# Kernel optimization log

Measured on AMD Instinct MI355X. Metric: run time of the kernel, lower is better.

## Reference

```python
import jax, jax.numpy as jnp
import numpy as np

D_MODEL = 768
N_HEAD = 8
D_K = D_MODEL // N_HEAD
SCALE = float(np.sqrt(D_K))
NEG = -1e9


def setup_inputs() -> dict:
    key = jax.random.key(0)
    ks = jax.random.split(key, 8)
    B, S = 2, 2048
    q = jax.random.normal(ks[0], (B, S, D_MODEL), dtype=jnp.float32)
    k = jax.random.normal(ks[1], (B, S, D_MODEL), dtype=jnp.float32)
    v = jax.random.normal(ks[2], (B, S, D_MODEL), dtype=jnp.float32)
    mask = jax.random.randint(ks[3], (B, 1, S, S), 0, 2, dtype=jnp.int32)
    # nn.Linear(d, d, bias=False) weights, stored as [in, out] for x @ W
    init = 1.0 / np.sqrt(D_MODEL)
    Wq = jax.random.uniform(ks[4], (D_MODEL, D_MODEL), jnp.float32, -init, init)
    Wk = jax.random.uniform(ks[5], (D_MODEL, D_MODEL), jnp.float32, -init, init)
    Wv = jax.random.uniform(ks[6], (D_MODEL, D_MODEL), jnp.float32, -init, init)
    Wo = jax.random.uniform(ks[7], (D_MODEL, D_MODEL), jnp.float32, -init, init)
    return {"query": q, "key": k, "value": v, "mask": mask,
            "Wq": Wq, "Wk": Wk, "Wv": Wv, "Wo": Wo}


def _split_heads(x):
    B, S, _ = x.shape
    return x.reshape(B, S, N_HEAD, D_K).transpose(0, 2, 1, 3)  # [B,H,S,Dk]


def reference(query, key, value, mask, Wq, Wk, Wv, Wo):
    Q = _split_heads(query @ Wq)
    K = _split_heads(key @ Wk)
    V = _split_heads(value @ Wv)
    logits = jnp.einsum('bhqd,bhkd->bhqk', Q, K) / SCALE  # [B,H,S,S]
    logits = jnp.where(mask == 0, NEG, logits)
    attn = jax.nn.softmax(logits, axis=-1)
    x = jnp.einsum('bhqk,bhkd->bhqd', attn, V)  # dropout=0 (eval)
    B, H, S, Dk = x.shape
    concat = x.transpose(0, 2, 1, 3).reshape(B, S, H * Dk)
    return concat @ Wo, attn
```

## Files before the change

### kernel.cpp

```cpp
#include <hip/hip_runtime.h>
#include <hip/hip_bf16.h>

typedef __bf16 bf16_t;
typedef __bf16 bf16x4 __attribute__((ext_vector_type(4)));
typedef __bf16 bf16x8 __attribute__((ext_vector_type(8)));
typedef float f32x4 __attribute__((ext_vector_type(4)));
typedef unsigned long long u64;

#define MFMA16(a, b, c) __builtin_amdgcn_mfma_f32_16x16x32_bf16(a, b, c, 0, 0, 0)

constexpr int B_ = 2, S_ = 2048, DM = 768, H_ = 8, DK = 96;
constexpr size_t OUT_ELEMS = 3145728;
constexpr float INV_SCALE = 0.10206207261596575f;
constexpr float NEGINF = -1e9f;

constexpr size_t QW_OFF = 0, KW_OFF = 6291456, VT_OFF = 12582912, WT_OFF = 18874368;
constexpr size_t XC_OFF = 23592960, MB_OFF = 29884416;

__global__ __launch_bounds__(256) void pack_mask(const int* __restrict__ mask,
                                                 u64* __restrict__ bits) {
    const int row = blockIdx.x;
    const int tid = threadIdx.x, lane = tid & 63, wv = tid >> 6;
    const int* mrow = mask + (size_t)row * S_;
    u64* brow = bits + (size_t)row * 32;
#pragma unroll
    for (int p = 0; p < 8; ++p) {
        const u64 b = __ballot(mrow[p * 256 + wv * 64 + lane] != 0);
        if (lane == 0) brow[p * 4 + wv] = b;
    }
}

__global__ __launch_bounds__(256) void prep_w(const float* __restrict__ w0,
                                              const float* __restrict__ w1,
                                              const float* __restrict__ w2,
                                              const float* __restrict__ w3,
                                              bf16_t* __restrict__ wt) {
    __shared__ float tile[32][33];
    const int z = blockIdx.z;
    const float* W = (z == 0) ? w0 : (z == 1) ? w1 : (z == 2) ? w2 : w3;
    bf16_t* out = wt + (size_t)z * DM * DM;
    const int k0 = blockIdx.x * 32, n0 = blockIdx.y * 32;
    const int tx = threadIdx.x & 31, ty = threadIdx.x >> 5;
#pragma unroll
    for (int i = 0; i < 32; i += 8) tile[ty + i][tx] = W[(size_t)(k0 + ty + i) * DM + n0 + tx];
    __syncthreads();
#pragma unroll
    for (int i = 0; i < 32; i += 8) out[(size_t)(n0 + ty + i) * DM + k0 + tx] = (bf16_t)tile[tx][ty + i];
}

template <int AMODE>
__device__ __forceinline__ void gemm_core(const void* __restrict__ Aglob,
                                          const bf16_t* __restrict__ Bt,
                                          int gm0, int gn0, f32x4 acc[4][4]) {
    __shared__ bf16_t As[128][40];
    __shared__ bf16_t Bs[128][40];
    const int tid = threadIdx.x, lane = tid & 63, wid = tid >> 6;
    const int wr = wid >> 1, wc = wid & 1;
    const int l15 = lane & 15, lq = lane >> 4;
    for (int kt = 0; kt < DM / 32; ++kt) {
        if (AMODE == 0) {
            const float* A = (const float*)Aglob;
#pragma unroll
            for (int p = 0; p < 4; ++p) {
                const int row = p * 32 + (tid >> 3);
                const int c4 = (tid & 7) * 4;
                const float4 vv = *(const float4*)&A[(size_t)(gm0 + row) * DM + kt * 32 + c4];
                As[row][c4 + 0] = (bf16_t)vv.x; As[row][c4 + 1] = (bf16_t)vv.y;
                As[row][c4 + 2] = (bf16_t)vv.z; As[row][c4 + 3] = (bf16_t)vv.w;
            }
        } else {
            const bf16_t* A = (const bf16_t*)Aglob;
#pragma unroll
            for (int p = 0; p < 2; ++p) {
                const int row = p * 64 + (tid >> 2);
                const int c8 = (tid & 3) * 8;
                *(uint4*)&As[row][c8] = *(const uint4*)&A[(size_t)(gm0 + row) * DM + kt * 32 + c8];
            }
        }
#pragma unroll
        for (int p = 0; p < 2; ++p) {
            const int row = p * 64 + (tid >> 2);
            const int c8 = (tid & 3) * 8;
            *(uint4*)&Bs[row][c8] = *(const uint4*)&Bt[(size_t)(gn0 + row) * DM + kt * 32 + c8];
        }
        __syncthreads();
        bf16x8 af[4], bfr[4];
#pragma unroll
        for (int i = 0; i < 4; ++i) af[i] = *(const bf16x8*)&As[wr * 64 + i * 16 + l15][lq * 8];
#pragma unroll
        for (int i = 0; i < 4; ++i) bfr[i] = *(const bf16x8*)&Bs[wc * 64 + i * 16 + l15][lq * 8];
#pragma unroll
        for (int i = 0; i < 4; ++i)
#pragma unroll
            for (int j = 0; j < 4; ++j) acc[i][j] = MFMA16(af[i], bfr[j], acc[i][j]);
        __syncthreads();
    }
}

__global__ __launch_bounds__(256) void qkv_gemm(const float* __restrict__ Xq,
                                                const float* __restrict__ Xk,
                                                const float* __restrict__ Xv,
                                                const bf16_t* __restrict__ Wt,
                                                bf16_t* __restrict__ Qw,
                                                bf16_t* __restrict__ Kw,
                                                bf16_t* __restrict__ Vt) {
    const int z = blockIdx.z;
    const float* A = (z == 0) ? Xq : (z == 1) ? Xk : Xv;
    const bf16_t* Bz = Wt + (size_t)z * DM * DM;
    const int gm0 = blockIdx.x * 128, gn0 = blockIdx.y * 128;
    f32x4 acc[4][4];
#pragma unroll
    for (int i = 0; i < 4; ++i)
#pragma unroll
        for (int j = 0; j < 4; ++j) acc[i][j] = (f32x4){0.f, 0.f, 0.f, 0.f};
    gemm_core<0>(A, Bz, gm0, gn0, acc);
    const int lane = threadIdx.x & 63, wid = threadIdx.x >> 6;
    const int wr = wid >> 1, wc = wid & 1;
#pragma unroll
    for (int i = 0; i < 4; ++i)
#pragma unroll
        for (int j = 0; j < 4; ++j)
#pragma unroll
            for (int e = 0; e < 4; ++e) {
                const int gm = gm0 + wr * 64 + i * 16 + (lane >> 4) * 4 + e;
                const int gn = gn0 + wc * 64 + j * 16 + (lane & 15);
                const int b = gm >> 11, s = gm & 2047;
                const int h = gn / DK, dk = gn % DK;
                const float val = acc[i][j][e];
                if (z == 2)
                    Vt[(((size_t)b * H_ + h) * DK + dk) * S_ + s] = (bf16_t)val;
                else {
                    bf16_t* dst = (z == 0) ? Qw : Kw;
                    dst[(((size_t)b * H_ + h) * S_ + s) * DK + dk] = (bf16_t)val;
                }
            }
}

__global__ __launch_bounds__(512, 4) void attn_fused(const bf16_t* __restrict__ Qw,
                                                     const bf16_t* __restrict__ Kw,
                                                     const u64* __restrict__ mbits,
                                                     const bf16_t* __restrict__ Vt,
                                                     float* __restrict__ attnf,
                                                     bf16_t* __restrict__ Xc) {
    const int bh = blockIdx.y;
    const int q0 = blockIdx.x * 16;
    const int tid = threadIdx.x, lane = tid & 63, w = tid >> 6;
    const int l15 = lane & 15, lq = lane >> 4;
    const int b = bh >> 3, h = bh & 7;

    __shared__ float redmax[8][16];
    __shared__ float redsum[8][16];
    __shared__ bf16_t p_lds[8][16][40];
    __shared__ float pv_part[8][16][96];

    bf16x8 aq[3];
    {
        const bf16_t* qb = Qw + ((size_t)bh * S_ + q0 + l15) * DK + lq * 8;
#pragma unroll
        for (int kk = 0; kk < 3; ++kk) aq[kk] = *(const bf16x8*)(qb + kk * 32);
    }
    const bf16_t* kbase = Kw + (size_t)bh * S_ * DK + lq * 8;
    const u64* mb = mbits + ((size_t)b * S_ + q0 + l15) * 32;

    f32x4 accs[16];
    float rmax = -1e30f;
#pragma unroll
    for (int tg = 0; tg < 4; ++tg) {
        const u64 mw = mb[w * 4 + tg];
#pragma unroll
        for (int dt = 0; dt < 4; ++dt) {
            const int t = tg * 4 + dt;
            const int kt = w * 16 + t;
            const bf16_t* kr = kbase + (size_t)(kt * 16 + l15) * DK;
            f32x4 acc = {0.f, 0.f, 0.f, 0.f};
            acc = MFMA16(*(const bf16x8*)(kr), aq[0], acc);
            acc = MFMA16(*(const bf16x8*)(kr + 32), aq[1], acc);
            acc = MFMA16(*(const bf16x8*)(kr + 64), aq[2], acc);
            const int sh = dt * 16 + lq * 4;
            const unsigned bm = (unsigned)(mw >> sh) & 0xFu;
#pragma unroll
            for (int e = 0; e < 4; ++e) {
                const float lv = ((bm >> e) & 1u) ? acc[e] * INV_SCALE : NEGINF;
                acc[e] = lv;
                rmax = fmaxf(rmax, lv);
            }
            accs[t] = acc;
        }
    }
    rmax = fmaxf(rmax, __shfl_xor(rmax, 16, 64));
    rmax = fmaxf(rmax, __shfl_xor(rmax, 32, 64));
    if (lane < 16) redmax[w][lane] = rmax;
    __syncthreads();
    float gmax = redmax[0][l15];
#pragma unroll
    for (int i = 1; i < 8; ++i) gmax = fmaxf(gmax, redmax[i][l15]);

    float rsum = 0.f;
#pragma unroll
    for (int t = 0; t < 16; ++t)
#pragma unroll
        for (int e = 0; e < 4; ++e) {
            const float ev = __expf(accs[t][e] - gmax);
            accs[t][e] = ev;
            rsum += ev;
        }
    rsum += __shfl_xor(rsum, 16, 64);
    rsum += __shfl_xor(rsum, 32, 64);
    if (lane < 16) redsum[w][lane] = rsum;
    __syncthreads();
    float ssum = redsum[0][l15];
#pragma unroll
    for (int i = 1; i < 8; ++i) ssum += redsum[i][l15];
    const float inv = 1.0f / ssum;

    f32x4 acc6[6];
#pragma unroll
    for (int f = 0; f < 6; ++f) acc6[f] = (f32x4){0.f, 0.f, 0.f, 0.f};
    float* arow = attnf + ((size_t)bh * S_ + q0 + l15) * S_ + w * 256;
    const bf16_t* vbase = Vt + (size_t)bh * DK * S_ + lq * 8;

#pragma unroll
    for (int u = 0; u < 8; ++u) {
#pragma unroll
        for (int half = 0; half < 2; ++half) {
            const int t = 2 * u + half;
            bf16x4 nb;
#pragma unroll
            for (int e = 0; e < 4; ++e) nb[e] = (bf16_t)(accs[t][e] * inv);
            float4 st;
            st.x = (float)nb[0]; st.y = (float)nb[1]; st.z = (float)nb[2]; st.w = (float)nb[3];
            *(float4*)(arow + t * 16 + lq * 4) = st;
            *(bf16x4*)&p_lds[w][l15][half * 16 + lq * 4] = nb;
        }
        asm volatile("s_waitcnt lgkmcnt(0)" ::: "memory");
        const bf16x8 pa = *(const bf16x8*)&p_lds[w][l15][lq * 8];
        const int k0 = w * 256 + u * 32;
#pragma unroll
        for (int f = 0; f < 6; ++f) {
            const bf16x8 vb = *(const bf16x8*)(vbase + (size_t)(f * 16 + l15) * S_ + k0);
            acc6[f] = MFMA16(pa, vb, acc6[f]);
        }
    }

#pragma unroll
    for (int f = 0; f < 6; ++f)
#pragma unroll
        for (int e = 0; e < 4; ++e) pv_part[w][lq * 4 + e][f * 16 + l15] = acc6[f][e];
    __syncthreads();
    for (int i = tid; i < 16 * 96; i += 512) {
        const int row = i / 96, col = i % 96;
        float s = pv_part[0][row][col];
#pragma unroll
        for (int j = 1; j < 8; ++j) s += pv_part[j][row][col];
        Xc[((size_t)b * S_ + q0 + row) * DM + h * DK + col] = (bf16_t)s;
    }
}

__global__ __launch_bounds__(256) void out_gemm(const bf16_t* __restrict__ Xc,
                                                const bf16_t* __restrict__ Wot,
                                                float* __restrict__ outf) {
    const int gm0 = blockIdx.x * 128, gn0 = blockIdx.y * 128;
    f32x4 acc[4][4];
#pragma unroll
    for (int i = 0; i < 4; ++i)
#pragma unroll
        for (int j = 0; j < 4; ++j) acc[i][j] = (f32x4){0.f, 0.f, 0.f, 0.f};
    gemm_core<1>(Xc, Wot, gm0, gn0, acc);
    const int lane = threadIdx.x & 63, wid = threadIdx.x >> 6;
    const int wr = wid >> 1, wc = wid & 1;
#pragma unroll
    for (int i = 0; i < 4; ++i)
#pragma unroll
        for (int j = 0; j < 4; ++j)
#pragma unroll
            for (int e = 0; e < 4; ++e) {
                const int gm = gm0 + wr * 64 + i * 16 + (lane >> 4) * 4 + e;
                const int gn = gn0 + wc * 64 + j * 16 + (lane & 15);
                outf[(size_t)gm * DM + gn] = (float)(bf16_t)acc[i][j][e];
            }
}

extern "C" void kernel_launch(void* const* d_in, const int* in_sizes, int n_in,
                              void* d_out, int out_size, void* d_ws, size_t ws_size,
                              hipStream_t stream) {
    const float* q = (const float*)d_in[0];
    const float* k = (const float*)d_in[1];
    const float* v = (const float*)d_in[2];
    const int* mask = (const int*)d_in[3];
    const float* Wq = (const float*)d_in[4];
    const float* Wk = (const float*)d_in[5];
    const float* Wv = (const float*)d_in[6];
    const float* Wo = (const float*)d_in[7];

    float* outf = (float*)d_out;
    float* attnf = (float*)d_out + OUT_ELEMS;

    char* ws = (char*)d_ws;
    bf16_t* Qw = (bf16_t*)(ws + QW_OFF);
    bf16_t* Kw = (bf16_t*)(ws + KW_OFF);
    bf16_t* Vt = (bf16_t*)(ws + VT_OFF);
    bf16_t* Wt = (bf16_t*)(ws + WT_OFF);
    bf16_t* Xc = (bf16_t*)(ws + XC_OFF);
    u64* mbits = (u64*)(ws + MB_OFF);

    prep_w<<<dim3(24, 24, 4), 256, 0, stream>>>(Wq, Wk, Wv, Wo, Wt);
    pack_mask<<<B_ * S_, 256, 0, stream>>>(mask, mbits);
    qkv_gemm<<<dim3(32, 6, 3), 256, 0, stream>>>(q, k, v, Wt, Qw, Kw, Vt);
    attn_fused<<<dim3(128, 16), 512, 0, stream>>>(Qw, Kw, mbits, Vt, attnf, Xc);
    out_gemm<<<dim3(32, 6), 256, 0, stream>>>(Xc, Wt + (size_t)3 * DM * DM, outf);
}
```

Measured before the change: 248.5 us.

## Halve PV partial LDS buffer via tree reduction and raise attention occupancy

Replaces the 8-way shared-memory partial-sum buffer for the P·V accumulators with a 3-step tree reduction that needs only half the LDS. The launch bound hint for the fused attention kernel is raised from 4 to 8 blocks per SM. The aim is to fit more blocks per compute unit by cutting shared memory and pressuring the compiler toward fewer registers. The cost is extra barriers, a serialized reduction tail where only one wave writes the output, and possible register spills under the tighter bound.

```diff
diff --git a/kernel.cpp b/kernel.cpp
--- a/kernel.cpp
+++ b/kernel.cpp
@@ -136,7 +136,7 @@
             }
 }
 
-__global__ __launch_bounds__(512, 4) void attn_fused(const bf16_t* __restrict__ Qw,
+__global__ __launch_bounds__(512, 8) void attn_fused(const bf16_t* __restrict__ Qw,
                                                      const bf16_t* __restrict__ Kw,
                                                      const u64* __restrict__ mbits,
                                                      const bf16_t* __restrict__ Vt,
@@ -151,7 +151,7 @@
     __shared__ float redmax[8][16];
     __shared__ float redsum[8][16];
     __shared__ bf16_t p_lds[8][16][40];
-    __shared__ float pv_part[8][16][96];
+    __shared__ float pv_part[4][16][96];
 
     bf16x8 aq[3];
     {
@@ -242,17 +242,49 @@
         }
     }
 
-#pragma unroll
-    for (int f = 0; f < 6; ++f)
-#pragma unroll
-        for (int e = 0; e < 4; ++e) pv_part[w][lq * 4 + e][f * 16 + l15] = acc6[f][e];
-    __syncthreads();
-    for (int i = tid; i < 16 * 96; i += 512) {
-        const int row = i / 96, col = i % 96;
-        float s = pv_part[0][row][col];
-#pragma unroll
-        for (int j = 1; j < 8; ++j) s += pv_part[j][row][col];
-        Xc[((size_t)b * S_ + q0 + row) * DM + h * DK + col] = (bf16_t)s;
+    if (w >= 4) {
+#pragma unroll
+        for (int f = 0; f < 6; ++f)
+#pragma unroll
+            for (int e = 0; e < 4; ++e) pv_part[w - 4][lq * 4 + e][f * 16 + l15] = acc6[f][e];
+    }
+    __syncthreads();
+    if (w < 4) {
+#pragma unroll
+        for (int f = 0; f < 6; ++f)
+#pragma unroll
+            for (int e = 0; e < 4; ++e) acc6[f][e] += pv_part[w][lq * 4 + e][f * 16 + l15];
+    }
+    __syncthreads();
+    if (w >= 2 && w < 4) {
+#pragma unroll
+        for (int f = 0; f < 6; ++f)
+#pragma unroll
+            for (int e = 0; e < 4; ++e) pv_part[w - 2][lq * 4 + e][f * 16 + l15] = acc6[f][e];
+    }
+    __syncthreads();
+    if (w < 2) {
+#pragma unroll
+        for (int f = 0; f < 6; ++f)
+#pragma unroll
+            for (int e = 0; e < 4; ++e) acc6[f][e] += pv_part[w][lq * 4 + e][f * 16 + l15];
+    }
+    __syncthreads();
+    if (w == 1) {
+#pragma unroll
+        for (int f = 0; f < 6; ++f)
+#pragma unroll
+            for (int e = 0; e < 4; ++e) pv_part[0][lq * 4 + e][f * 16 + l15] = acc6[f][e];
+    }
+    __syncthreads();
+    if (w == 0) {
+#pragma unroll
+        for (int f = 0; f < 6; ++f)
+#pragma unroll
+            for (int e = 0; e < 4; ++e) {
+                const float s = acc6[f][e] + pv_part[0][lq * 4 + e][f * 16 + l15];
+                Xc[((size_t)b * S_ + q0 + lq * 4 + e) * DM + h * DK + f * 16 + l15] = (bf16_t)s;
+            }
     }
 }
 
```

New measurement: 412.2 us. 65.9% more time.
